# Performance work log

Hardware: AMD Instinct MI355X
Metric: run time of the kernel (lower is better)

Reference implementation:

```python
import jax, jax.numpy as jnp
import numpy as np

N, P, T, K = 20000, 5, 16, 3
IN, H, O = 150, 64, 128


def setup_inputs() -> dict:
    key = jax.random.key(0)
    k1, k2, k3, k4, k5 = jax.random.split(key, 5)
    x = jax.random.normal(k1, (N, IN), dtype=jnp.float32)
    conn_idx = jax.random.randint(k2, (N, P, T, K), 0, N, dtype=jnp.int32)
    conn_w = jax.random.uniform(k3, (N, P, T, K), dtype=jnp.float32)
    # learned params
    W1 = jax.random.normal(k4, (H, IN), dtype=jnp.float32) * 0.05   # linear_1 (no bias)
    Wg = jax.random.normal(k5, (O, H, P, T), dtype=jnp.float32) * 0.05  # geodesic conv weight
    bg = jnp.zeros((O,), dtype=jnp.float32)                          # geodesic conv bias
    return {"x": x, "conn_idx": conn_idx, "conn_w": conn_w, "W1": W1, "Wg": Wg, "bg": bg}


def reference(x, conn_idx, conn_w, W1, Wg, bg):
    # Linear + ReLU: [N, H]
    h = jax.nn.relu(x @ W1.T)
    # Geodesic patch gather: interpolate vertex features into P x T bins
    g = jnp.take(h, conn_idx, axis=0)                 # [N, P, T, K, H]
    patches = jnp.einsum('nptk,nptkh->npth', conn_w, g)  # [N, P, T, H]
    # Geodesic convolution: contract patch bins and channels
    out = jnp.einsum('npth,ohpt->no', patches, Wg) + bg  # [N, O]
    # L2 normalize per vertex
    norm = jnp.linalg.norm(out, axis=-1, keepdims=True)
    return out / norm
```

## Files before the change

### kernel.cpp

```cpp
#include <hip/hip_runtime.h>
#include <hip/hip_fp16.h>

#define NV   20000
#define KK   3
#define INF  150
#define HH   64
#define OO   128
#define PT   80
#define KTOT 5120
#define NB   64
#define RS   72
#define CB   (NB * RS)
#define XS   168
#define NBIN 20

typedef _Float16 fh8 __attribute__((ext_vector_type(8)));
typedef __attribute__((ext_vector_type(4))) float f32x4;

__device__ __forceinline__ unsigned short f2h(float f) {
    return __half_as_ushort(__float2half(f));
}
__device__ __forceinline__ float h2f(unsigned short u) {
    return __half2float(__ushort_as_half(u));
}
__device__ __forceinline__ _Float16 u2h(unsigned short u) {
    union { unsigned short s; _Float16 h; } c; c.s = u; return c.h;
}

__global__ __launch_bounds__(256) void prep_kernel(
    const float* __restrict__ Wg, const float* __restrict__ x,
    const float* __restrict__ W1, unsigned short* __restrict__ W2,
    unsigned short* __restrict__ hb) {
    __shared__ __align__(16) unsigned char smem[32256];
    const int tid = threadIdx.x;

    if (blockIdx.x < 128) {
        float* lds = (float*)smem;
        const int o = blockIdx.x;
        const float* src = Wg + o * KTOT;
        for (int t = tid; t < KTOT; t += 256) {
            int h = t / 80, bin = t - h * 80;
            lds[h * 81 + bin] = src[t];
        }
        __syncthreads();
        for (int t = tid; t < KTOT; t += 256) {
            W2[(t >> 5) * 4096 + o * 32 + (t & 31)] =
                f2h(lds[(t & 63) * 81 + (t >> 6)]);
        }
        return;
    }

    unsigned short* xs = (unsigned short*)smem;
    unsigned short* ws = xs + 32 * XS;
    const int n0 = (blockIdx.x - 128) * 32;

    for (int e = tid; e < 32 * INF; e += 256) {
        int r = e / INF, c = e - r * INF;
        xs[r * XS + c] = f2h(x[n0 * INF + e]);
    }
    for (int e = tid; e < 32 * 18; e += 256) {
        int r = e / 18, c = e - r * 18;
        xs[r * XS + 150 + c] = 0;
    }
    for (int e = tid; e < 64 * INF; e += 256) {
        int r = e / INF, c = e - r * INF;
        ws[r * XS + c] = f2h(W1[e]);
    }
    for (int e = tid; e < 64 * 18; e += 256) {
        int r = e / 18, c = e - r * 18;
        ws[r * XS + 150 + c] = 0;
    }
    __syncthreads();

    const int wv   = tid >> 6;
    const int lane = tid & 63;
    const int q    = lane >> 4;
    const int r16  = lane & 15;
    const int o0   = wv * 16;

    f32x4 acc0 = {0.f, 0.f, 0.f, 0.f};
    f32x4 acc1 = acc0;
    #pragma unroll
    for (int s = 0; s < 5; s++) {
        const int kb = s * 32 + q * 8;
        fh8 a0 = *(const fh8*)(xs + r16 * XS + kb);
        fh8 a1 = *(const fh8*)(xs + (16 + r16) * XS + kb);
        fh8 b  = *(const fh8*)(ws + (o0 + r16) * XS + kb);
        acc0 = __builtin_amdgcn_mfma_f32_16x16x32_f16(a0, b, acc0, 0, 0, 0);
        acc1 = __builtin_amdgcn_mfma_f32_16x16x32_f16(a1, b, acc1, 0, 0, 0);
    }
    #pragma unroll
    for (int r = 0; r < 4; r++) {
        float v0 = acc0[r] > 0.f ? acc0[r] : 0.f;
        float v1 = acc1[r] > 0.f ? acc1[r] : 0.f;
        hb[(n0 + q * 4 + r) * HH + o0 + r16]      = f2h(v0);
        hb[(n0 + 16 + q * 4 + r) * HH + o0 + r16] = f2h(v1);
    }
}

__global__ __launch_bounds__(512, 6) void geo_kernel(
    const int*   __restrict__ conn_idx, const float* __restrict__ conn_w,
    const unsigned short* __restrict__ W2, const unsigned short* __restrict__ hb,
    float* __restrict__ out, unsigned short* __restrict__ parts) {
    __shared__ __align__(16) unsigned short pch[2 * CB];
    __shared__ unsigned short ci[NB * 60];
    __shared__ unsigned short cw[NB * 60];

    const int tid  = threadIdx.x;
    const int ks   = blockIdx.x & 3;
    const int n0   = (blockIdx.x >> 2) * NB;
    const int wv   = tid >> 6;
    const int lane = tid & 63;
    const int q    = lane >> 4;
    const int r16  = lane & 15;
    const int mp   = wv & 1;
    const int op   = wv >> 1;
    const int j8   = tid & 7;
    const int vg   = tid >> 3;
    const int bbase = ks * NBIN;
    const int Sbase = ks * 40;

    for (int e = tid; e < NB * 60; e += 512) {
        const int r = e / 60, c = e - r * 60;
        const int v = n0 + r;
        if (v < NV) {
            const int g = v * (PT * KK) + bbase * KK + c;
            ci[e] = (unsigned short)conn_idx[g];
            cw[e] = f2h(conn_w[g]);
        } else {
            ci[e] = 0;
            cw[e] = 0;
        }
    }

    f32x4 acc00 = {0.f, 0.f, 0.f, 0.f};
    f32x4 acc01 = acc00, acc10 = acc00, acc11 = acc00;

    fh8 hv0, hv1, hv2;
    unsigned short w0u, w1u, w2u;

    auto loadg = [&](int cc) {
        const int base = vg * 60 + cc * 3;
        const int i0 = ci[base], i1 = ci[base + 1], i2 = ci[base + 2];
        w0u = cw[base]; w1u = cw[base + 1]; w2u = cw[base + 2];
        hv0 = *(const fh8*)(hb + i0 * HH + j8 * 8);
        hv1 = *(const fh8*)(hb + i1 * HH + j8 * 8);
        hv2 = *(const fh8*)(hb + i2 * HH + j8 * 8);
    };
    auto cwr = [&](unsigned short* buf) {
        const _Float16 w0 = u2h(w0u), w1 = u2h(w1u), w2 = u2h(w2u);
        const fh8 W0 = {w0, w0, w0, w0, w0, w0, w0, w0};
        const fh8 W1v = {w1, w1, w1, w1, w1, w1, w1, w1};
        const fh8 W2v = {w2, w2, w2, w2, w2, w2, w2, w2};
        fh8 r = hv0 * W0 + hv1 * W1v + hv2 * W2v;
        *(fh8*)(buf + vg * RS + j8 * 8) = r;
    };
    auto mfmaph = [&](const unsigned short* buf, int cc) {
        #pragma unroll
        for (int s = 0; s < 2; s++) {
            const int S  = Sbase + cc * 2 + s;
            const int ao = s * 32 + q * 8;
            fh8 a0 = *(const fh8*)(buf + (mp * 32 + r16) * RS + ao);
            fh8 a1 = *(const fh8*)(buf + (mp * 32 + 16 + r16) * RS + ao);
            fh8 b0 = *(const fh8*)(W2 + S * 4096 + ((op * 2 + 0) * 16 + r16) * 32 + q * 8);
            fh8 b1 = *(const fh8*)(W2 + S * 4096 + ((op * 2 + 1) * 16 + r16) * 32 + q * 8);
            acc00 = __builtin_amdgcn_mfma_f32_16x16x32_f16(a0, b0, acc00, 0, 0, 0);
            acc01 = __builtin_amdgcn_mfma_f32_16x16x32_f16(a0, b1, acc01, 0, 0, 0);
            acc10 = __builtin_amdgcn_mfma_f32_16x16x32_f16(a1, b0, acc10, 0, 0, 0);
            acc11 = __builtin_amdgcn_mfma_f32_16x16x32_f16(a1, b1, acc11, 0, 0, 0);
        }
    };

    __syncthreads();

    loadg(0);
    cwr(pch);
    __syncthreads();

    for (int cc = 0; cc < NBIN; cc++) {
        if (cc + 1 < NBIN) loadg(cc + 1);
        mfmaph(&pch[(cc & 1) * CB], cc);
        if (cc + 1 < NBIN) cwr(&pch[((cc + 1) & 1) * CB]);
        __syncthreads();
    }

    if (ks == 0) {
        #pragma unroll
        for (int a = 0; a < 2; a++) {
            const int rb = n0 + (2 * mp + a) * 16 + q * 4;
            #pragma unroll
            for (int r = 0; r < 4; r++) {
                if (rb + r < NV) {
                    out[(rb + r) * OO + (2 * op + 0) * 16 + r16] = a ? acc10[r] : acc00[r];
                    out[(rb + r) * OO + (2 * op + 1) * 16 + r16] = a ? acc11[r] : acc01[r];
                }
            }
        }
    } else {
        unsigned short* pp = parts + (ks - 1) * (NV * OO);
        #pragma unroll
        for (int a = 0; a < 2; a++) {
            const int rb = n0 + (2 * mp + a) * 16 + q * 4;
            #pragma unroll
            for (int r = 0; r < 4; r++) {
                if (rb + r < NV) {
                    pp[(rb + r) * OO + (2 * op + 0) * 16 + r16] = f2h(a ? acc10[r] : acc00[r]);
                    pp[(rb + r) * OO + (2 * op + 1) * 16 + r16] = f2h(a ? acc11[r] : acc01[r]);
                }
            }
        }
    }
}

__global__ __launch_bounds__(256) void norm_kernel(
    float* __restrict__ out, const unsigned short* __restrict__ parts,
    const float* __restrict__ bg) {
    const int tid = threadIdx.x;
    const int n   = blockIdx.x * 32 + (tid >> 3);
    const int l   = tid & 7;
    float v[16];
    float s = 0.f;
    #pragma unroll
    for (int i = 0; i < 16; i++) {
        const int o = i * 8 + l;
        const int e = n * OO + o;
        v[i] = out[e] + h2f(parts[e]) + h2f(parts[NV * OO + e]) +
               h2f(parts[2 * NV * OO + e]) + bg[o];
        s += v[i] * v[i];
    }
    for (int off = 4; off; off >>= 1) s += __shfl_down(s, off, 8);
    const float r = rsqrtf(__shfl(s, 0, 8));
    #pragma unroll
    for (int i = 0; i < 16; i++)
        out[n * OO + i * 8 + l] = v[i] * r;
}

extern "C" void kernel_launch(void* const* d_in, const int* in_sizes, int n_in,
                              void* d_out, int out_size, void* d_ws, size_t ws_size,
                              hipStream_t stream) {
    const float* x        = (const float*)d_in[0];
    const int*   conn_idx = (const int*)  d_in[1];
    const float* conn_w   = (const float*)d_in[2];
    const float* W1       = (const float*)d_in[3];
    const float* Wg       = (const float*)d_in[4];
    const float* bg       = (const float*)d_in[5];
    float*       out      = (float*)d_out;

    unsigned short* W2    = (unsigned short*)d_ws;
    unsigned short* hb    = W2 + OO * KTOT;
    unsigned short* parts = hb + NV * HH;

    hipLaunchKernelGGL(prep_kernel, dim3(128 + NV / 32), dim3(256), 0, stream,
                       Wg, x, W1, W2, hb);
    hipLaunchKernelGGL(geo_kernel, dim3(4 * 313), dim3(512), 0, stream,
                       conn_idx, conn_w, W2, hb, out, parts);
    hipLaunchKernelGGL(norm_kernel, dim3(NV / 32), dim3(256), 0, stream,
                       out, parts, bg);
}
```

Before: 180.5 us.

## Halve geo_kernel block to 256 threads with 4x2 MFMA tiles per wave

Shrinks the geodesic conv block from 512 to 256 threads. Each wave now covers all 64 rows and two 16-column output tiles, so every W2 B-fragment load is reused across four MFMAs instead of two. Each thread gathers two vertices' patches per bin. Connectivity index and weight are packed into one 16-byte LDS record per vertex-bin, so a single vector load replaces six scalar LDS reads. The cost is fewer threads to hide gather latency and more accumulator registers per thread, which can lower occupancy.

```diff
diff --git a/kernel.cpp b/kernel.cpp
--- a/kernel.cpp
+++ b/kernel.cpp
@@ -16,6 +16,7 @@
 
 typedef _Float16 fh8 __attribute__((ext_vector_type(8)));
 typedef __attribute__((ext_vector_type(4))) float f32x4;
+typedef __attribute__((ext_vector_type(8))) unsigned short u16x8;
 
 __device__ __forceinline__ unsigned short f2h(float f) {
     return __half_as_ushort(__float2half(f));
@@ -98,13 +99,12 @@
     }
 }
 
-__global__ __launch_bounds__(512, 6) void geo_kernel(
+__global__ __launch_bounds__(256, 4) void geo_kernel(
     const int*   __restrict__ conn_idx, const float* __restrict__ conn_w,
     const unsigned short* __restrict__ W2, const unsigned short* __restrict__ hb,
     float* __restrict__ out, unsigned short* __restrict__ parts) {
     __shared__ __align__(16) unsigned short pch[2 * CB];
-    __shared__ unsigned short ci[NB * 60];
-    __shared__ unsigned short cw[NB * 60];
+    __shared__ __align__(16) unsigned short cp[NB * NBIN * 8];
 
     const int tid  = threadIdx.x;
     const int ks   = blockIdx.x & 3;
@@ -113,61 +113,74 @@
     const int lane = tid & 63;
     const int q    = lane >> 4;
     const int r16  = lane & 15;
-    const int mp   = wv & 1;
-    const int op   = wv >> 1;
     const int j8   = tid & 7;
-    const int vg   = tid >> 3;
+    const int v0   = tid >> 3;
     const int bbase = ks * NBIN;
     const int Sbase = ks * 40;
 
-    for (int e = tid; e < NB * 60; e += 512) {
-        const int r = e / 60, c = e - r * 60;
-        const int v = n0 + r;
-        if (v < NV) {
-            const int g = v * (PT * KK) + bbase * KK + c;
-            ci[e] = (unsigned short)conn_idx[g];
-            cw[e] = f2h(conn_w[g]);
-        } else {
-            ci[e] = 0;
-            cw[e] = 0;
-        }
-    }
-
-    f32x4 acc00 = {0.f, 0.f, 0.f, 0.f};
-    f32x4 acc01 = acc00, acc10 = acc00, acc11 = acc00;
-
-    fh8 hv0, hv1, hv2;
-    unsigned short w0u, w1u, w2u;
+    for (int e = tid; e < NB * NBIN; e += 256) {
+        const int v = e / NBIN, cc = e - v * NBIN;
+        const int vv = n0 + v;
+        u16x8 pk = {0, 0, 0, 0, 0, 0, 0, 0};
+        if (vv < NV) {
+            const int g = vv * (PT * KK) + (bbase + cc) * KK;
+            pk[0] = (unsigned short)conn_idx[g];
+            pk[1] = (unsigned short)conn_idx[g + 1];
+            pk[2] = (unsigned short)conn_idx[g + 2];
+            pk[3] = f2h(conn_w[g]);
+            pk[4] = f2h(conn_w[g + 1]);
+            pk[5] = f2h(conn_w[g + 2]);
+        }
+        *(u16x8*)(cp + e * 8) = pk;
+    }
+
+    f32x4 acc[4][2];
+    #pragma unroll
+    for (int m = 0; m < 4; m++) {
+        acc[m][0] = (f32x4){0.f, 0.f, 0.f, 0.f};
+        acc[m][1] = (f32x4){0.f, 0.f, 0.f, 0.f};
+    }
+
+    u16x8 pa, pb;
+    fh8   hva0, hva1, hva2, hvb0, hvb1, hvb2;
 
     auto loadg = [&](int cc) {
-        const int base = vg * 60 + cc * 3;
-        const int i0 = ci[base], i1 = ci[base + 1], i2 = ci[base + 2];
-        w0u = cw[base]; w1u = cw[base + 1]; w2u = cw[base + 2];
-        hv0 = *(const fh8*)(hb + i0 * HH + j8 * 8);
-        hv1 = *(const fh8*)(hb + i1 * HH + j8 * 8);
-        hv2 = *(const fh8*)(hb + i2 * HH + j8 * 8);
+        pa = *(const u16x8*)(cp + (v0 * NBIN + cc) * 8);
+        pb = *(const u16x8*)(cp + ((v0 + 32) * NBIN + cc) * 8);
+        hva0 = *(const fh8*)(hb + (int)pa[0] * HH + j8 * 8);
+        hva1 = *(const fh8*)(hb + (int)pa[1] * HH + j8 * 8);
+        hva2 = *(const fh8*)(hb + (int)pa[2] * HH + j8 * 8);
+        hvb0 = *(const fh8*)(hb + (int)pb[0] * HH + j8 * 8);
+        hvb1 = *(const fh8*)(hb + (int)pb[1] * HH + j8 * 8);
+        hvb2 = *(const fh8*)(hb + (int)pb[2] * HH + j8 * 8);
     };
     auto cwr = [&](unsigned short* buf) {
-        const _Float16 w0 = u2h(w0u), w1 = u2h(w1u), w2 = u2h(w2u);
-        const fh8 W0 = {w0, w0, w0, w0, w0, w0, w0, w0};
-        const fh8 W1v = {w1, w1, w1, w1, w1, w1, w1, w1};
-        const fh8 W2v = {w2, w2, w2, w2, w2, w2, w2, w2};
-        fh8 r = hv0 * W0 + hv1 * W1v + hv2 * W2v;
-        *(fh8*)(buf + vg * RS + j8 * 8) = r;
+        const _Float16 a0 = u2h(pa[3]), a1 = u2h(pa[4]), a2 = u2h(pa[5]);
+        const _Float16 b0 = u2h(pb[3]), b1 = u2h(pb[4]), b2 = u2h(pb[5]);
+        const fh8 A0 = {a0, a0, a0, a0, a0, a0, a0, a0};
+        const fh8 A1 = {a1, a1, a1, a1, a1, a1, a1, a1};
+        const fh8 A2 = {a2, a2, a2, a2, a2, a2, a2, a2};
+        const fh8 B0 = {b0, b0, b0, b0, b0, b0, b0, b0};
+        const fh8 B1 = {b1, b1, b1, b1, b1, b1, b1, b1};
+        const fh8 B2 = {b2, b2, b2, b2, b2, b2, b2, b2};
+        fh8 ra = hva0 * A0 + hva1 * A1 + hva2 * A2;
+        fh8 rb = hvb0 * B0 + hvb1 * B1 + hvb2 * B2;
+        *(fh8*)(buf + v0 * RS + j8 * 8)        = ra;
+        *(fh8*)(buf + (v0 + 32) * RS + j8 * 8) = rb;
     };
     auto mfmaph = [&](const unsigned short* buf, int cc) {
         #pragma unroll
         for (int s = 0; s < 2; s++) {
             const int S  = Sbase + cc * 2 + s;
             const int ao = s * 32 + q * 8;
-            fh8 a0 = *(const fh8*)(buf + (mp * 32 + r16) * RS + ao);
-            fh8 a1 = *(const fh8*)(buf + (mp * 32 + 16 + r16) * RS + ao);
-            fh8 b0 = *(const fh8*)(W2 + S * 4096 + ((op * 2 + 0) * 16 + r16) * 32 + q * 8);
-            fh8 b1 = *(const fh8*)(W2 + S * 4096 + ((op * 2 + 1) * 16 + r16) * 32 + q * 8);
-            acc00 = __builtin_amdgcn_mfma_f32_16x16x32_f16(a0, b0, acc00, 0, 0, 0);
-            acc01 = __builtin_amdgcn_mfma_f32_16x16x32_f16(a0, b1, acc01, 0, 0, 0);
-            acc10 = __builtin_amdgcn_mfma_f32_16x16x32_f16(a1, b0, acc10, 0, 0, 0);
-            acc11 = __builtin_amdgcn_mfma_f32_16x16x32_f16(a1, b1, acc11, 0, 0, 0);
+            fh8 bf0 = *(const fh8*)(W2 + S * 4096 + ((wv * 2 + 0) * 16 + r16) * 32 + q * 8);
+            fh8 bf1 = *(const fh8*)(W2 + S * 4096 + ((wv * 2 + 1) * 16 + r16) * 32 + q * 8);
+            #pragma unroll
+            for (int m = 0; m < 4; m++) {
+                fh8 af = *(const fh8*)(buf + (m * 16 + r16) * RS + ao);
+                acc[m][0] = __builtin_amdgcn_mfma_f32_16x16x32_f16(af, bf0, acc[m][0], 0, 0, 0);
+                acc[m][1] = __builtin_amdgcn_mfma_f32_16x16x32_f16(af, bf1, acc[m][1], 0, 0, 0);
+            }
         }
     };
 
@@ -186,26 +199,26 @@
 
     if (ks == 0) {
         #pragma unroll
-        for (int a = 0; a < 2; a++) {
-            const int rb = n0 + (2 * mp + a) * 16 + q * 4;
+        for (int m = 0; m < 4; m++) {
+            const int rb = n0 + m * 16 + q * 4;
             #pragma unroll
             for (int r = 0; r < 4; r++) {
                 if (rb + r < NV) {
-                    out[(rb + r) * OO + (2 * op + 0) * 16 + r16] = a ? acc10[r] : acc00[r];
-                    out[(rb + r) * OO + (2 * op + 1) * 16 + r16] = a ? acc11[r] : acc01[r];
+                    out[(rb + r) * OO + (wv * 2 + 0) * 16 + r16] = acc[m][0][r];
+                    out[(rb + r) * OO + (wv * 2 + 1) * 16 + r16] = acc[m][1][r];
                 }
             }
         }
     } else {
         unsigned short* pp = parts + (ks - 1) * (NV * OO);
         #pragma unroll
-        for (int a = 0; a < 2; a++) {
-            const int rb = n0 + (2 * mp + a) * 16 + q * 4;
+        for (int m = 0; m < 4; m++) {
+            const int rb = n0 + m * 16 + q * 4;
             #pragma unroll
             for (int r = 0; r < 4; r++) {
                 if (rb + r < NV) {
-                    pp[(rb + r) * OO + (2 * op + 0) * 16 + r16] = f2h(a ? acc10[r] : acc00[r]);
-                    pp[(rb + r) * OO + (2 * op + 1) * 16 + r16] = f2h(a ? acc11[r] : acc01[r]);
+                    pp[(rb + r) * OO + (wv * 2 + 0) * 16 + r16] = f2h(acc[m][0][r]);
+                    pp[(rb + r) * OO + (wv * 2 + 1) * 16 + r16] = f2h(acc[m][1][r]);
                 }
             }
         }
@@ -252,7 +265,7 @@
 
     hipLaunchKernelGGL(prep_kernel, dim3(128 + NV / 32), dim3(256), 0, stream,
                        Wg, x, W1, W2, hb);
-    hipLaunchKernelGGL(geo_kernel, dim3(4 * 313), dim3(512), 0, stream,
+    hipLaunchKernelGGL(geo_kernel, dim3(4 * 313), dim3(256), 0, stream,
                        conn_idx, conn_w, W2, hb, out, parts);
     hipLaunchKernelGGL(norm_kernel, dim3(NV / 32), dim3(256), 0, stream,
                        out, parts, bg);
```

Measured after the change: 174.0 us. 3.6% less time.
